# Kernel tuning notes

Hardware: AMD Instinct MI355X
Metric: run time of the kernel (lower is better)

## Reference

```python
import jax, jax.numpy as jnp
import numpy as np

B, L, N, D, TOPK, OUT_V = 32, 512, 1024, 64, 20, 1024
BN_EPS = 1e-5
NEG_SLOPE = 0.2


def setup_inputs() -> dict:
    key = jax.random.key(0)
    ks = jax.random.split(key, 8)
    s = lambda k, shape, sc=0.05: jax.random.normal(k, shape, jnp.float32) * sc
    return {
        "x_enc": jax.random.normal(ks[0], (B, L, N), jnp.float32),
        "emb": s(ks[1], (N, D), 0.1),          # nn.Embedding(variate, d_model).weight
        "lin_W": s(ks[2], (L, D)),              # GraphLayer.lin (no bias)
        "att_i": s(ks[3], (D,)),
        "att_j": s(ks[4], (D,)),
        "att_em_i": s(ks[5], (D,)),
        "att_em_j": s(ks[6], (D,)),
        "gnn_b": jnp.zeros((D,), jnp.float32),  # GraphLayer bias (concat=False)
        "g1": jnp.ones((D,), jnp.float32), "b1": jnp.zeros((D,), jnp.float32),   # GNNLayer.bn
        "g2": jnp.ones((D,), jnp.float32), "b2": jnp.zeros((D,), jnp.float32),   # bn_outlayer_in
        "out_W": s(ks[7], (D, 1)), "out_b": jnp.zeros((1,), jnp.float32),        # OutLayer Linear(d_model, 1)
    }


def _forward(x_enc, emb, lin_W, att_i, att_j, att_em_i, att_em_j,
             gnn_b, g1, b1, g2, b2, out_W, out_b):
    # --- LIN: LayerNorm(input_len, eps=0, no affine) over time, first OUT_V variates ---
    xv = jnp.transpose(x_enc[:, :, :OUT_V], (0, 2, 1))          # [B, OUT_V, L]
    xv = (xv - xv.mean(-1, keepdims=True)) / jnp.sqrt(xv.var(-1, keepdims=True))
    x_enc = x_enc.at[:, :, :OUT_V].set(jnp.transpose(xv, (0, 2, 1)))
    x_enc = jnp.nan_to_num(x_enc, nan=0.0, posinf=0.0, neginf=0.0)

    gt = x_enc[:, -1:, :OUT_V]                                   # [B, 1, OUT_V]
    enc = x_enc.at[:, -1:, :OUT_V].set(0.0)

    # x = enc.transpose(0,1).view(-1, L)  (faithful to original reshape)
    x = jnp.transpose(enc, (1, 0, 2)).reshape(-1, L)             # [B*N, L]

    # --- dynamic top-k cosine-similarity graph (embeddings detached) ---
    w = jax.lax.stop_gradient(emb)
    nrm = jnp.linalg.norm(w, axis=-1)
    cos = (w @ w.T) / (nrm[:, None] * nrm[None, :])              # [N, N]
    topk_idx = jax.lax.top_k(cos, TOPK)[1]                       # [N, TOPK]
    src = topk_idx.reshape(-1)                                   # gated_j (source)
    dst = jnp.repeat(jnp.arange(N), TOPK)                        # gated_i (target)

    offs = (jnp.arange(B) * N)[:, None]
    src_b = (src[None, :] + offs).reshape(-1)                    # [B*N*TOPK]
    dst_b = (dst[None, :] + offs).reshape(-1)

    # remove_self_loops (mask out) then add_self_loops for all B*N nodes
    num_nodes = B * N
    self_mask = jnp.concatenate([src_b == dst_b, jnp.zeros(num_nodes, bool)])
    src_all = jnp.concatenate([src_b, jnp.arange(num_nodes)])
    dst_all = jnp.concatenate([dst_b, jnp.arange(num_nodes)])

    # --- GraphLayer (GAT-style, heads=1, concat=False) ---
    h = x @ lin_W                                                # [B*N, D]
    all_emb = jnp.tile(emb, (B, 1))                              # [B*N, D]

    logit = (h[dst_all] @ att_i + all_emb[dst_all] @ att_em_i
             + h[src_all] @ att_j + all_emb[src_all] @ att_em_j)  # [E]
    logit = jnp.where(logit >= 0, logit, NEG_SLOPE * logit)      # leaky_relu(0.2)
    logit = jnp.where(self_mask, -jnp.inf, logit)

    seg_max = jax.ops.segment_max(logit, dst_all, num_segments=num_nodes)
    expv = jnp.where(self_mask, 0.0, jnp.exp(logit - seg_max[dst_all]))
    denom = jax.ops.segment_sum(expv, dst_all, num_segments=num_nodes)
    alpha = expv / denom[dst_all]

    out = jax.ops.segment_sum(h[src_all] * alpha[:, None], dst_all,
                              num_segments=num_nodes) + gnn_b    # [B*N, D]

    # GNNLayer: BatchNorm1d(D) (batch stats) + ReLU
    out = (out - out.mean(0)) / jnp.sqrt(out.var(0) + BN_EPS) * g1 + b1
    out = jax.nn.relu(out)

    # --- combine with embedding, bn_outlayer_in, OutLayer ---
    xg = out.reshape(B, N, D) * emb[None]                        # [B, N, D]
    xg = jnp.transpose(xg, (0, 2, 1))                            # [B, D, N]
    mu = xg.mean((0, 2), keepdims=True)
    var = xg.var((0, 2), keepdims=True)
    xg = (xg - mu) / jnp.sqrt(var + BN_EPS) * g2[None, :, None] + b2[None, :, None]
    xg = jnp.transpose(jax.nn.relu(xg), (0, 2, 1))               # [B, N, D]

    o = xg @ out_W + out_b                                       # [B, N, 1]
    o = jnp.transpose(o, (0, 2, 1))                              # [B, 1, N]
    return o[:, :, :OUT_V], gt


def reference(x_enc, emb, lin_W, att_i, att_j, att_em_i, att_em_j,
              gnn_b, g1, b1, g2, b2, out_W, out_b):
    return _forward(x_enc, emb, lin_W, att_i, att_j, att_em_i, att_em_j,
                    gnn_b, g1, b1, g2, b2, out_W, out_b)
```

## Files before the change

kernel.cpp:

```cpp
#include <hip/hip_runtime.h>
#include <stdint.h>

#define BB 32
#define LL 512
#define NNODES 1024
#define DD 64
#define TOPK 20
#define NTOT (BB*NNODES)
#define LNSZ (LL*NNODES)

typedef short short8 __attribute__((ext_vector_type(8)));
typedef float floatx4 __attribute__((ext_vector_type(4)));

__device__ __forceinline__ float bf2f(unsigned short u){
    union { unsigned int i; float f; } x; x.i = ((unsigned int)u) << 16; return x.f;
}
__device__ __forceinline__ unsigned short f2bf(float f){
    union { float f; unsigned int i; } x; x.f = f;
    unsigned int u = x.i;
    return (unsigned short)((u + 0x7FFFu + ((u >> 16) & 1u)) >> 16);
}
__device__ __forceinline__ void unpack2(unsigned int w, float& lo, float& hi){
    union { unsigned int i; float f; } a, b;
    a.i = w << 16; b.i = w & 0xFFFF0000u;
    lo = a.f; hi = b.f;
}
__device__ __forceinline__ float ldf(const void* p, int i, int isf){
    return isf ? ((const float*)p)[i] : bf2f(((const unsigned short*)p)[i]);
}
__device__ __forceinline__ int detect_isf(const void* xv){
    const unsigned short* x = (const unsigned short*)xv;
    int lane = threadIdx.x & 63;
    unsigned int idx = ((unsigned)lane * 131071u) & 0x7FFFFFu;
    float v = bf2f(x[idx * 2]);
    float a = fabsf(v);
    int crazy = (!(a <= 1e3f)) || (v != 0.f && a < 1e-6f);
    unsigned long long m = __ballot(crazy);
    return __popcll(m) > 16;
}

__global__ void __launch_bounds__(256) k01_prep(const void* x, const void* lw, unsigned short* wt,
                                                const void* emb, const void* aemi, const void* aemj,
                                                float* eai, float* eaj, float* embT, float* rsqm,
                                                float* part, float* stats){
    int isf = detect_isf(x);
    int t = threadIdx.x;
    if (blockIdx.x == 0) stats[t] = 0.f;
    if (blockIdx.x < 128){
        int id = blockIdx.x * 256 + t;
        int k = id >> 6, d = id & 63;
        unsigned short w = isf ? f2bf(((const float*)lw)[id]) : ((const unsigned short*)lw)[id];
        wt[d * 512 + k] = w;
        {
            int j = id;
            int dd = j >> 10, m = j & 1023;
            embT[j] = ldf(emb, m * 64 + dd, isf);
            j = id + 32768;
            dd = j >> 10; m = j & 1023;
            embT[j] = ldf(emb, m * 64 + dd, isf);
        }
        if (id < 1024){
            int n = id;
            float s1 = 0.f, s2 = 0.f;
            for (int dd = 0; dd < 64; dd++){
                float e = ldf(emb, n * 64 + dd, isf);
                s1 += e * ldf(aemi, dd, isf);
                s2 += e * ldf(aemj, dd, isf);
            }
            eai[n] = s1; eaj[n] = s2;
            float sq = 0.f;
            if (!isf){
                const uint4* pm = (const uint4*)((const unsigned short*)emb + n * 64);
                #pragma unroll
                for (int i = 0; i < 8; i++){
                    uint4 ww = pm[i];
                    float a0,a1,a2,a3,a4,a5,a6,a7;
                    unpack2(ww.x,a0,a1); unpack2(ww.y,a2,a3); unpack2(ww.z,a4,a5); unpack2(ww.w,a6,a7);
                    sq += a0*a0 + a1*a1 + a2*a2 + a3*a3 + a4*a4 + a5*a5 + a6*a6 + a7*a7;
                }
            } else {
                const float4* pm = (const float4*)((const float*)emb + n * 64);
                #pragma unroll
                for (int i = 0; i < 16; i++){
                    float4 ww = pm[i];
                    sq += ww.x*ww.x + ww.y*ww.y + ww.z*ww.z + ww.w*ww.w;
                }
            }
            rsqm[n] = rsqrtf(sq);
        }
    }
    int b = blockIdx.x >> 4, lq = blockIdx.x & 15;
    int n0 = t * 4;
    size_t base = (size_t)b * LNSZ + (size_t)(lq * 32) * NNODES + n0;
    float s0=0,s1=0,s2=0,s3=0,q0=0,q1=0,q2=0,q3=0;
    if (isf){
        const float* p = (const float*)x + base;
        for (int i = 0; i < 32; i++){
            float4 w = *(const float4*)p;
            s0+=w.x; q0+=w.x*w.x; s1+=w.y; q1+=w.y*w.y;
            s2+=w.z; q2+=w.z*w.z; s3+=w.w; q3+=w.w*w.w;
            p += NNODES;
        }
    } else {
        const unsigned short* p = (const unsigned short*)x + base;
        for (int i = 0; i < 32; i++){
            uint2 w = *(const uint2*)p;
            float a,bv,c,d2;
            unpack2(w.x, a, bv); unpack2(w.y, c, d2);
            s0+=a; q0+=a*a; s1+=bv; q1+=bv*bv; s2+=c; q2+=c*c; s3+=d2; q3+=d2*d2;
            p += NNODES;
        }
    }
    int v = b * NNODES + n0;
    float2* pp = (float2*)part;
    pp[(size_t)v*16 + lq]       = make_float2(s0,q0);
    pp[(size_t)(v+1)*16 + lq]   = make_float2(s1,q1);
    pp[(size_t)(v+2)*16 + lq]   = make_float2(s2,q2);
    pp[(size_t)(v+3)*16 + lq]   = make_float2(s3,q3);
}

__global__ void __launch_bounds__(256) k13_topk(const void* emb, const float* embT, const float* rsqm,
                                                int* topk, const void* x, const float* part,
                                                float* mr, float* outp){
    __shared__ float enf[64];
    __shared__ float n2s;
    __shared__ float crow[1024];
    int isf = detect_isf(x);
    int wave = threadIdx.x >> 6, lane = threadIdx.x & 63;
    int n = blockIdx.x;
    if (blockIdx.x < 128){
        int v = blockIdx.x * 256 + threadIdx.x;
        const float2* pp = (const float2*)part + (size_t)v * 16;
        float s = 0.f, q = 0.f;
        for (int i = 0; i < 16; i++){ float2 w = pp[i]; s += w.x; q += w.y; }
        float mean = s * (1.f/512.f);
        float var  = q * (1.f/512.f) - mean * mean;
        float rstd = var > 0.f ? rsqrtf(var) : 0.f;
        ((float2*)mr)[v] = make_float2(mean, rstd);
        int b = v >> 10, nn = v & 1023;
        float xv = ldf(x, (int)((size_t)b * LNSZ + (size_t)511 * NNODES + nn), isf);
        outp[NTOT + v] = (xv - mean) * rstd;
    }
    if (wave == 0){
        float e = ldf(emb, n * 64 + lane, isf);
        enf[lane] = e;
        float p1 = e * e;
        #pragma unroll
        for (int m = 1; m < 64; m <<= 1) p1 += __shfl_xor(p1, m, 64);
        if (lane == 0) n2s = p1;
    }
    __syncthreads();
    float rn_own = rsqrtf(n2s);
    const float* en = enf;
    int mb = wave * 256 + lane * 4;
    float dot0 = 0.f, dot1 = 0.f, dot2 = 0.f, dot3 = 0.f;
    if (!isf){
        #pragma unroll
        for (int i = 0; i < 8; i++){
            float4 a0 = *(const float4*)(embT + (i*8+0)*1024 + mb);
            float4 a1 = *(const float4*)(embT + (i*8+1)*1024 + mb);
            float4 a2 = *(const float4*)(embT + (i*8+2)*1024 + mb);
            float4 a3 = *(const float4*)(embT + (i*8+3)*1024 + mb);
            float4 a4 = *(const float4*)(embT + (i*8+4)*1024 + mb);
            float4 a5 = *(const float4*)(embT + (i*8+5)*1024 + mb);
            float4 a6 = *(const float4*)(embT + (i*8+6)*1024 + mb);
            float4 a7 = *(const float4*)(embT + (i*8+7)*1024 + mb);
            const float* e8 = en + i * 8;
            dot0 += e8[0]*a0.x + e8[1]*a1.x + e8[2]*a2.x + e8[3]*a3.x
                  + e8[4]*a4.x + e8[5]*a5.x + e8[6]*a6.x + e8[7]*a7.x;
            dot1 += e8[0]*a0.y + e8[1]*a1.y + e8[2]*a2.y + e8[3]*a3.y
                  + e8[4]*a4.y + e8[5]*a5.y + e8[6]*a6.y + e8[7]*a7.y;
            dot2 += e8[0]*a0.z + e8[1]*a1.z + e8[2]*a2.z + e8[3]*a3.z
                  + e8[4]*a4.z + e8[5]*a5.z + e8[6]*a6.z + e8[7]*a7.z;
            dot3 += e8[0]*a0.w + e8[1]*a1.w + e8[2]*a2.w + e8[3]*a3.w
                  + e8[4]*a4.w + e8[5]*a5.w + e8[6]*a6.w + e8[7]*a7.w;
        }
    } else {
        #pragma unroll
        for (int i = 0; i < 16; i++){
            float4 a0 = *(const float4*)(embT + (i*4+0)*1024 + mb);
            float4 a1 = *(const float4*)(embT + (i*4+1)*1024 + mb);
            float4 a2 = *(const float4*)(embT + (i*4+2)*1024 + mb);
            float4 a3 = *(const float4*)(embT + (i*4+3)*1024 + mb);
            const float* e4 = en + i * 4;
            dot0 += e4[0]*a0.x + e4[1]*a1.x + e4[2]*a2.x + e4[3]*a3.x;
            dot1 += e4[0]*a0.y + e4[1]*a1.y + e4[2]*a2.y + e4[3]*a3.y;
            dot2 += e4[0]*a0.z + e4[1]*a1.z + e4[2]*a2.z + e4[3]*a3.z;
            dot3 += e4[0]*a0.w + e4[1]*a1.w + e4[2]*a2.w + e4[3]*a3.w;
        }
    }
    crow[mb+0] = dot0 * rn_own * rsqm[mb+0];
    crow[mb+1] = dot1 * rn_own * rsqm[mb+1];
    crow[mb+2] = dot2 * rn_own * rsqm[mb+2];
    crow[mb+3] = dot3 * rn_own * rsqm[mb+3];
    __syncthreads();
    if (wave != 0) return;
    float va[16];
    #pragma unroll
    for (int ii = 0; ii < 16; ii++) va[ii] = crow[ii * 64 + lane];
    for (int k = 0; k < TOPK; k++){
        float t8[8]; int x8[8];
        #pragma unroll
        for (int j = 0; j < 8; j++){
            bool c = va[2*j+1] > va[2*j];
            t8[j] = c ? va[2*j+1] : va[2*j]; x8[j] = c ? 2*j+1 : 2*j;
        }
        #pragma unroll
        for (int j = 0; j < 4; j++){
            bool c = t8[2*j+1] > t8[2*j];
            t8[j] = c ? t8[2*j+1] : t8[2*j]; x8[j] = c ? x8[2*j+1] : x8[2*j];
        }
        #pragma unroll
        for (int j = 0; j < 2; j++){
            bool c = t8[2*j+1] > t8[2*j];
            t8[j] = c ? t8[2*j+1] : t8[2*j]; x8[j] = c ? x8[2*j+1] : x8[2*j];
        }
        bool c0 = t8[1] > t8[0];
        float bv = c0 ? t8[1] : t8[0]; int bi = c0 ? x8[1] : x8[0];
        int bm = bi * 64 + lane;
        #pragma unroll
        for (int s = 1; s < 64; s <<= 1){
            float ov = __shfl_xor(bv, s, 64);
            int   om = __shfl_xor(bm, s, 64);
            bool u = (ov > bv) || (ov == bv && om < bm);
            bv = u ? ov : bv; bm = u ? om : bm;
        }
        if (lane == 0) topk[n * TOPK + k] = bm;
        int evi = bm >> 6;
        bool own = ((bm & 63) == lane);
        #pragma unroll
        for (int ii = 0; ii < 16; ii++)
            va[ii] = (own && ii == evi) ? -__builtin_inff() : va[ii];
    }
}

__global__ void __launch_bounds__(256) k2_gemm_h(const void* x, const unsigned short* wt,
                                                const float* mr, unsigned short* hb,
                                                const void* atti, const void* attj,
                                                const float* eai, const float* eaj,
                                                float* ai, float* aj){
    __shared__ unsigned short A_l[64 * 136];
    __shared__ unsigned short W_l[64 * 136];
    __shared__ float4 colp4[256];
    int isf = detect_isf(x);
    int t = threadIdx.x;
    int q = blockIdx.x & 63, mtile = blockIdx.x >> 6;
    int b = q >> 1, nbase = (q & 1) * 512;
    size_t xbase = (size_t)b * LNSZ + nbase;

    colp4[t] = ((const float4*)mr)[q * 256 + t];

    int wave = t >> 6, lane = t & 63;
    int quad = lane >> 4, lcol = lane & 15;
    floatx4 acc[4];
    for (int j = 0; j < 4; j++) acc[j] = (floatx4){0.f,0.f,0.f,0.f};
    __syncthreads();

    for (int kc = 0; kc < 4; kc++){
        for (int i = 0; i < 4; i++){
            int id = i * 256 + t;
            int l = id >> 4, c16 = id & 15;
            int lg = mtile * 64 + l;
            uint4 o;
            if (lg == 511){
                o = make_uint4(0u, 0u, 0u, 0u);
            } else {
                size_t ofs = xbase + (size_t)lg * NNODES + kc * 128 + c16 * 8;
                float e0,e1,e2,e3,e4,e5,e6,e7;
                if (isf){
                    const float4* px = (const float4*)((const float*)x + ofs);
                    float4 wa = px[0], wb = px[1];
                    e0=wa.x; e1=wa.y; e2=wa.z; e3=wa.w; e4=wb.x; e5=wb.y; e6=wb.z; e7=wb.w;
                } else {
                    uint4 w = *(const uint4*)((const unsigned short*)x + ofs);
                    unpack2(w.x,e0,e1); unpack2(w.y,e2,e3); unpack2(w.z,e4,e5); unpack2(w.w,e6,e7);
                }
                int f4b = kc * 64 + c16 * 4;
                float4 pA = colp4[f4b+0], pB = colp4[f4b+1], pC = colp4[f4b+2], pD = colp4[f4b+3];
                e0 = (e0 - pA.x) * pA.y;  e1 = (e1 - pA.z) * pA.w;
                e2 = (e2 - pB.x) * pB.y;  e3 = (e3 - pB.z) * pB.w;
                e4 = (e4 - pC.x) * pC.y;  e5 = (e5 - pC.z) * pC.w;
                e6 = (e6 - pD.x) * pD.y;  e7 = (e7 - pD.z) * pD.w;
                o.x = (unsigned)f2bf(e0) | ((unsigned)f2bf(e1) << 16);
                o.y = (unsigned)f2bf(e2) | ((unsigned)f2bf(e3) << 16);
                o.z = (unsigned)f2bf(e4) | ((unsigned)f2bf(e5) << 16);
                o.w = (unsigned)f2bf(e6) | ((unsigned)f2bf(e7) << 16);
            }
            *(uint4*)&A_l[l * 136 + c16 * 8] = o;
        }
        for (int i = 0; i < 4; i++){
            int id = i * 256 + t;
            int dd = id >> 4, c16 = id & 15;
            uint4 w = *(const uint4*)(wt + dd * 512 + kc * 128 + c16 * 8);
            *(uint4*)&W_l[dd * 136 + c16 * 8] = w;
        }
        __syncthreads();
        for (int ks = 0; ks < 4; ks++){
            short8 af, bfr[4];
            af = *(const short8*)&A_l[(wave * 16 + lcol) * 136 + ks * 32 + quad * 8];
            for (int tc = 0; tc < 4; tc++)
                bfr[tc] = *(const short8*)&W_l[(tc * 16 + lcol) * 136 + ks * 32 + quad * 8];
            for (int tc = 0; tc < 4; tc++)
                acc[tc] = __builtin_amdgcn_mfma_f32_16x16x32_bf16(af, bfr[tc], acc[tc], 0, 0, 0);
        }
        __syncthreads();
    }
    float aw[4], jw[4];
    #pragma unroll
    for (int tc = 0; tc < 4; tc++){
        int dcol = tc * 16 + lcol;
        aw[tc] = ldf(atti, dcol, isf);
        jw[tc] = ldf(attj, dcol, isf);
    }
    #pragma unroll
    for (int r = 0; r < 4; r++){
        float pi = 0.f, pj = 0.f;
        #pragma unroll
        for (int tc = 0; tc < 4; tc++){
            float hv = acc[tc][r];
            pi += hv * aw[tc];
            pj += hv * jw[tc];
        }
        #pragma unroll
        for (int s = 1; s < 16; s <<= 1){
            pi += __shfl_xor(pi, s, 64);
            pj += __shfl_xor(pj, s, 64);
        }
        if (lcol == 0){
            int lrow = wave * 16 + quad * 4 + r;
            int row = (mtile * 64 + lrow) * 64 + q;
            int n = row & 1023;
            ai[row] = pi + eai[n];
            aj[row] = pj + eaj[n];
        }
    }
    for (int tc = 0; tc < 4; tc++){
        int dcol = tc * 16 + lcol;
        for (int r = 0; r < 4; r++){
            int lrow = wave * 16 + quad * 4 + r;
            int row = (mtile * 64 + lrow) * 64 + q;
            hb[(size_t)row * 64 + dcol] = f2bf(acc[tc][r]);
        }
    }
}

__global__ void __launch_bounds__(256) k5_attn(const unsigned short* hb, const float* ai, const float* aj,
                                               const int* topk, const void* gnn_b, float* out, const void* x){
    int isf = detect_isf(x);
    int wave = threadIdx.x >> 6, lane = threadIdx.x & 63;
    float gb = ldf(gnn_b, lane, isf);
    int v = blockIdx.x * 4 + wave;
    int n = v & 1023, bbase = v & ~1023;
    int srcv; bool valid;
    if (lane < TOPK){
        int id = topk[n * TOPK + lane];
        srcv = bbase | id;
        valid = (id != n);
    } else if (lane == TOPK){
        srcv = v; valid = true;
    } else { srcv = v; valid = false; }
    float l = ai[v] + aj[srcv];
    l = (l >= 0.f) ? l : 0.2f * l;
    if (!valid) l = -__builtin_inff();
    float m = l;
    #pragma unroll
    for (int s = 1; s < 64; s <<= 1){ float o = __shfl_xor(m, s, 64); m = fmaxf(m, o); }
    float ev = valid ? __expf(l - m) : 0.f;
    float dsum = ev;
    #pragma unroll
    for (int s = 1; s < 64; s <<= 1) dsum += __shfl_xor(dsum, s, 64);
    float rd = 1.f / dsum;
    float acc = 0.f;
    #pragma unroll
    for (int j = 0; j <= TOPK; j++){
        float e = __shfl(ev, j, 64);
        int  sj = __shfl(srcv, j, 64);
        acc += e * bf2f(hb[(size_t)sj * 64 + lane]);
    }
    out[(size_t)v * 64 + lane] = acc * rd + gb;
}

__global__ void __launch_bounds__(256) k5b_stats(const float* out, float* stats1){
    __shared__ float bs[256], bq[256];
    int wave = threadIdx.x >> 6, lane = threadIdx.x & 63;
    int v0 = blockIdx.x * 128 + wave * 32;
    float ssum = 0.f, ssq = 0.f;
    for (int i = 0; i < 32; i++){
        float x = out[(size_t)(v0 + i) * 64 + lane];
        ssum += x; ssq += x * x;
    }
    bs[threadIdx.x] = ssum; bq[threadIdx.x] = ssq;
    __syncthreads();
    if (wave == 0){
        float s  = bs[lane] + bs[64+lane] + bs[128+lane] + bs[192+lane];
        float qq = bq[lane] + bq[64+lane] + bq[128+lane] + bq[192+lane];
        atomicAdd(&stats1[lane], s);
        atomicAdd(&stats1[64 + lane], qq);
    }
}

__global__ void __launch_bounds__(256) k6_stats2(const float* out, const float* stats1, const void* g1,
                                                 const void* b1, const void* emb,
                                                 float* stats2, const void* x){
    __shared__ float bs[256], bq[256];
    int isf = detect_isf(x);
    int wave = threadIdx.x >> 6, lane = threadIdx.x & 63;
    float mu   = stats1[lane] * (1.f/32768.f);
    float var  = stats1[64 + lane] * (1.f/32768.f) - mu * mu;
    float rstd = 1.f / sqrtf(var + 1e-5f);
    float g = ldf(g1, lane, isf), bb = ldf(b1, lane, isf);
    float ssum = 0.f, ssq = 0.f;
    int v0 = (blockIdx.x * 4 + wave) * 16;
    for (int i = 0; i < 16; i++){
        int v = v0 + i; int n = v & 1023;
        float xv = out[(size_t)v * 64 + lane];
        float y = fmaxf((xv - mu) * rstd * g + bb, 0.f);
        float z = y * ldf(emb, n * 64 + lane, isf);
        ssum += z; ssq += z * z;
    }
    bs[threadIdx.x] = ssum; bq[threadIdx.x] = ssq;
    __syncthreads();
    if (wave == 0){
        float s  = bs[lane] + bs[64+lane] + bs[128+lane] + bs[192+lane];
        float qq = bq[lane] + bq[64+lane] + bq[128+lane] + bq[192+lane];
        atomicAdd(&stats2[lane], s);
        atomicAdd(&stats2[64 + lane], qq);
    }
}

__global__ void __launch_bounds__(256) k7_out(const float* out, const float* stats1, const float* stats2,
                                              const void* g1, const void* b1,
                                              const void* g2, const void* b2,
                                              const void* emb, const void* outw,
                                              const void* outb, float* o, const void* x){
    int isf = detect_isf(x);
    int wave = threadIdx.x >> 6, lane = threadIdx.x & 63;
    float mu1   = stats1[lane] * (1.f/32768.f);
    float var1  = stats1[64 + lane] * (1.f/32768.f) - mu1 * mu1;
    float rstd1 = 1.f / sqrtf(var1 + 1e-5f);
    float g1v = ldf(g1, lane, isf), b1v = ldf(b1, lane, isf);
    float mu2   = stats2[lane] * (1.f/32768.f);
    float var2  = stats2[64 + lane] * (1.f/32768.f) - mu2 * mu2;
    float rstd2 = 1.f / sqrtf(var2 + 1e-5f);
    float g2v = ldf(g2, lane, isf), b2v = ldf(b2, lane, isf);
    float w = ldf(outw, lane, isf);
    float ob = ldf(outb, 0, isf);
    int v0 = (blockIdx.x * 4 + wave) * 16;
    for (int i = 0; i < 16; i++){
        int v = v0 + i; int n = v & 1023;
        float xv = out[(size_t)v * 64 + lane];
        float z = fmaxf((xv - mu1) * rstd1 * g1v + b1v, 0.f) * ldf(emb, n * 64 + lane, isf);
        float y = fmaxf((z - mu2) * rstd2 * g2v + b2v, 0.f);
        float p = y * w;
        for (int s = 1; s < 64; s <<= 1) p += __shfl_xor(p, s, 64);
        if (lane == 0) o[v] = p + ob;
    }
}

extern "C" void kernel_launch(void* const* d_in, const int* in_sizes, int n_in,
                              void* d_out, int out_size, void* d_ws, size_t ws_size,
                              hipStream_t stream){
    const void* x    = d_in[0];
    const void* emb  = d_in[1];
    const void* linW = d_in[2];
    const void* atti = d_in[3];
    const void* attj = d_in[4];
    const void* aemi = d_in[5];
    const void* aemj = d_in[6];
    const void* gnnb = d_in[7];
    const void* g1   = d_in[8];
    const void* b1   = d_in[9];
    const void* g2   = d_in[10];
    const void* b2   = d_in[11];
    const void* outw = d_in[12];
    const void* outb = d_in[13];
    float* o = (float*)d_out;

    char* w = (char*)d_ws;
    float*          mr    = (float*)(w + 0);
    unsigned short* wt    = (unsigned short*)(w + 262144);
    unsigned short* hb    = (unsigned short*)(w + 327680);
    float*          eai   = (float*)(w + 8716288);
    float*          eaj   = (float*)(w + 8720384);
    int*            topk  = (int*)(w + 8724480);
    float*          ai    = (float*)(w + 8806400);
    float*          aj    = (float*)(w + 8937472);
    float*          outg  = (float*)(w + 9068544);
    float*          part  = outg;
    float*          embT  = (float*)(w + 13262848);
    float*          rsqm  = (float*)(w + 13524992);
    float*          stats = (float*)(w + 17457152);

    hipLaunchKernelGGL(k01_prep, dim3(512),  dim3(256), 0, stream, x, linW, wt, emb, aemi, aemj,
                       eai, eaj, embT, rsqm, part, stats);
    hipLaunchKernelGGL(k13_topk, dim3(1024), dim3(256), 0, stream, emb, embT, rsqm, topk, x, part, mr, o);
    hipLaunchKernelGGL(k2_gemm_h, dim3(512), dim3(256), 0, stream, x, wt, mr, hb, atti, attj, eai, eaj, ai, aj);
    hipLaunchKernelGGL(k5_attn,  dim3(8192), dim3(256), 0, stream, hb, ai, aj, topk, gnnb, outg, x);
    hipLaunchKernelGGL(k5b_stats, dim3(256), dim3(256), 0, stream, outg, stats);
    hipLaunchKernelGGL(k6_stats2, dim3(512), dim3(256), 0, stream, outg, stats, g1, b1, emb, stats + 128, x);
    hipLaunchKernelGGL(k7_out,   dim3(512),  dim3(256), 0, stream, outg, stats, stats + 128,
                       g1, b1, g2, b2, emb, outw, outb, o, x);
}
```

Before: 233.4 us.

## Load GEMM fragments directly from global memory into registers, dropping LDS staging

The k2_gemm_h kernel no longer stages the normalized input tile and weight tile through shared memory with block barriers. Each lane now loads its own MFMA A fragment directly from global memory, applies the per-column normalization inline, and reads the B fragments directly from the weight array, with the loops fully unrolled. This removes LDS writes and reads and the __syncthreads barriers. In exchange, the weight tile is re-read from global/L2 by every wave rather than shared once per block, and the global access patterns are less coalesced, since each lane reads 8 contiguous elements from a different row.

```diff
diff --git a/kernel.cpp b/kernel.cpp
--- a/kernel.cpp
+++ b/kernel.cpp
@@ -239,33 +239,28 @@
                                                 const void* atti, const void* attj,
                                                 const float* eai, const float* eaj,
                                                 float* ai, float* aj){
-    __shared__ unsigned short A_l[64 * 136];
-    __shared__ unsigned short W_l[64 * 136];
-    __shared__ float4 colp4[256];
     int isf = detect_isf(x);
     int t = threadIdx.x;
     int q = blockIdx.x & 63, mtile = blockIdx.x >> 6;
     int b = q >> 1, nbase = (q & 1) * 512;
     size_t xbase = (size_t)b * LNSZ + nbase;
-
-    colp4[t] = ((const float4*)mr)[q * 256 + t];
-
     int wave = t >> 6, lane = t & 63;
     int quad = lane >> 4, lcol = lane & 15;
+    int lg = mtile * 64 + wave * 16 + lcol;
+    const float4* colp = (const float4*)mr + q * 256;
+
     floatx4 acc[4];
+    #pragma unroll
     for (int j = 0; j < 4; j++) acc[j] = (floatx4){0.f,0.f,0.f,0.f};
-    __syncthreads();
 
     for (int kc = 0; kc < 4; kc++){
-        for (int i = 0; i < 4; i++){
-            int id = i * 256 + t;
-            int l = id >> 4, c16 = id & 15;
-            int lg = mtile * 64 + l;
-            uint4 o;
+        short8 af[4];
+        #pragma unroll
+        for (int ks = 0; ks < 4; ks++){
             if (lg == 511){
-                o = make_uint4(0u, 0u, 0u, 0u);
+                af[ks] = (short8){0,0,0,0,0,0,0,0};
             } else {
-                size_t ofs = xbase + (size_t)lg * NNODES + kc * 128 + c16 * 8;
+                size_t ofs = xbase + (size_t)lg * NNODES + kc * 128 + ks * 32 + quad * 8;
                 float e0,e1,e2,e3,e4,e5,e6,e7;
                 if (isf){
                     const float4* px = (const float4*)((const float*)x + ofs);
@@ -275,35 +270,30 @@
                     uint4 w = *(const uint4*)((const unsigned short*)x + ofs);
                     unpack2(w.x,e0,e1); unpack2(w.y,e2,e3); unpack2(w.z,e4,e5); unpack2(w.w,e6,e7);
                 }
-                int f4b = kc * 64 + c16 * 4;
-                float4 pA = colp4[f4b+0], pB = colp4[f4b+1], pC = colp4[f4b+2], pD = colp4[f4b+3];
+                int f = kc * 64 + ks * 16 + quad * 4;
+                float4 pA = colp[f], pB = colp[f+1], pC = colp[f+2], pD = colp[f+3];
                 e0 = (e0 - pA.x) * pA.y;  e1 = (e1 - pA.z) * pA.w;
                 e2 = (e2 - pB.x) * pB.y;  e3 = (e3 - pB.z) * pB.w;
                 e4 = (e4 - pC.x) * pC.y;  e5 = (e5 - pC.z) * pC.w;
                 e6 = (e6 - pD.x) * pD.y;  e7 = (e7 - pD.z) * pD.w;
-                o.x = (unsigned)f2bf(e0) | ((unsigned)f2bf(e1) << 16);
-                o.y = (unsigned)f2bf(e2) | ((unsigned)f2bf(e3) << 16);
-                o.z = (unsigned)f2bf(e4) | ((unsigned)f2bf(e5) << 16);
-                o.w = (unsigned)f2bf(e6) | ((unsigned)f2bf(e7) << 16);
+                short8 a;
+                a[0] = (short)f2bf(e0); a[1] = (short)f2bf(e1);
+                a[2] = (short)f2bf(e2); a[3] = (short)f2bf(e3);
+                a[4] = (short)f2bf(e4); a[5] = (short)f2bf(e5);
+                a[6] = (short)f2bf(e6); a[7] = (short)f2bf(e7);
+                af[ks] = a;
             }
-            *(uint4*)&A_l[l * 136 + c16 * 8] = o;
-        }
-        for (int i = 0; i < 4; i++){
-            int id = i * 256 + t;
-            int dd = id >> 4, c16 = id & 15;
-            uint4 w = *(const uint4*)(wt + dd * 512 + kc * 128 + c16 * 8);
-            *(uint4*)&W_l[dd * 136 + c16 * 8] = w;
-        }
-        __syncthreads();
+        }
+        #pragma unroll
         for (int ks = 0; ks < 4; ks++){
-            short8 af, bfr[4];
-            af = *(const short8*)&A_l[(wave * 16 + lcol) * 136 + ks * 32 + quad * 8];
+            short8 bfr[4];
+            #pragma unroll
             for (int tc = 0; tc < 4; tc++)
-                bfr[tc] = *(const short8*)&W_l[(tc * 16 + lcol) * 136 + ks * 32 + quad * 8];
+                bfr[tc] = *(const short8*)(wt + (tc * 16 + lcol) * 512 + kc * 128 + ks * 32 + quad * 8);
+            #pragma unroll
             for (int tc = 0; tc < 4; tc++)
-                acc[tc] = __builtin_amdgcn_mfma_f32_16x16x32_bf16(af, bfr[tc], acc[tc], 0, 0, 0);
-        }
-        __syncthreads();
+                acc[tc] = __builtin_amdgcn_mfma_f32_16x16x32_bf16(af[ks], bfr[tc], acc[tc], 0, 0, 0);
+        }
     }
     float aw[4], jw[4];
     #pragma unroll
@@ -334,8 +324,10 @@
             aj[row] = pj + eaj[n];
         }
     }
+    #pragma unroll
     for (int tc = 0; tc < 4; tc++){
         int dcol = tc * 16 + lcol;
+        #pragma unroll
         for (int r = 0; r < 4; r++){
             int lrow = wave * 16 + quad * 4 + r;
             int row = (mtile * 64 + lrow) * 64 + q;
```

Result: slower. 248.1 us (+6.3%).

## Widen stats reduction grid, transpose partial layout, swizzle GEMM shared tiles

Applied to the files above, without the earlier changes.

The per-variate LayerNorm statistics pass now runs on twice as many blocks, with each thread reading 8 contiguous variates over 8 time steps. Partial sums go into a partition-major layout so both the writes and the reads in the topk kernel are coalesced. The GEMM kernel replaces its padded shared-memory tiles with XOR-swizzled uint4 tiles to avoid bank conflicts without padding, and unrolls its loops. The reducer now sums 64 partials instead of 16, and part moves to a separate workspace region, which assumes the workspace is large enough.

```diff
diff --git a/kernel.cpp b/kernel.cpp
--- a/kernel.cpp
+++ b/kernel.cpp
@@ -89,34 +89,46 @@
             rsqm[n] = rsqrtf(sq);
         }
     }
-    int b = blockIdx.x >> 4, lq = blockIdx.x & 15;
-    int n0 = t * 4;
-    size_t base = (size_t)b * LNSZ + (size_t)(lq * 32) * NNODES + n0;
-    float s0=0,s1=0,s2=0,s3=0,q0=0,q1=0,q2=0,q3=0;
+    int b = blockIdx.x >> 5, lq = blockIdx.x & 31;
+    int th = t & 127, rh = t >> 7;
+    int n0 = th * 8;
+    int l0 = lq * 16 + rh * 8;
+    size_t base = (size_t)b * LNSZ + (size_t)l0 * NNODES + n0;
+    float s0=0,s1=0,s2=0,s3=0,s4=0,s5=0,s6=0,s7=0;
+    float q0=0,q1=0,q2=0,q3=0,q4=0,q5=0,q6=0,q7=0;
     if (isf){
         const float* p = (const float*)x + base;
-        for (int i = 0; i < 32; i++){
-            float4 w = *(const float4*)p;
-            s0+=w.x; q0+=w.x*w.x; s1+=w.y; q1+=w.y*w.y;
-            s2+=w.z; q2+=w.z*w.z; s3+=w.w; q3+=w.w*w.w;
+        #pragma unroll
+        for (int i = 0; i < 8; i++){
+            float4 wa = *(const float4*)p;
+            float4 wb = *(const float4*)(p + 4);
+            s0+=wa.x; q0+=wa.x*wa.x; s1+=wa.y; q1+=wa.y*wa.y;
+            s2+=wa.z; q2+=wa.z*wa.z; s3+=wa.w; q3+=wa.w*wa.w;
+            s4+=wb.x; q4+=wb.x*wb.x; s5+=wb.y; q5+=wb.y*wb.y;
+            s6+=wb.z; q6+=wb.z*wb.z; s7+=wb.w; q7+=wb.w*wb.w;
             p += NNODES;
         }
     } else {
         const unsigned short* p = (const unsigned short*)x + base;
-        for (int i = 0; i < 32; i++){
-            uint2 w = *(const uint2*)p;
-            float a,bv,c,d2;
-            unpack2(w.x, a, bv); unpack2(w.y, c, d2);
-            s0+=a; q0+=a*a; s1+=bv; q1+=bv*bv; s2+=c; q2+=c*c; s3+=d2; q3+=d2*d2;
+        #pragma unroll
+        for (int i = 0; i < 8; i++){
+            uint4 w = *(const uint4*)p;
+            float e0,e1,e2,e3,e4,e5,e6,e7;
+            unpack2(w.x,e0,e1); unpack2(w.y,e2,e3); unpack2(w.z,e4,e5); unpack2(w.w,e6,e7);
+            s0+=e0; q0+=e0*e0; s1+=e1; q1+=e1*e1;
+            s2+=e2; q2+=e2*e2; s3+=e3; q3+=e3*e3;
+            s4+=e4; q4+=e4*e4; s5+=e5; q5+=e5*e5;
+            s6+=e6; q6+=e6*e6; s7+=e7; q7+=e7*e7;
             p += NNODES;
         }
     }
-    int v = b * NNODES + n0;
-    float2* pp = (float2*)part;
-    pp[(size_t)v*16 + lq]       = make_float2(s0,q0);
-    pp[(size_t)(v+1)*16 + lq]   = make_float2(s1,q1);
-    pp[(size_t)(v+2)*16 + lq]   = make_float2(s2,q2);
-    pp[(size_t)(v+3)*16 + lq]   = make_float2(s3,q3);
+    int pidx = lq * 2 + rh;
+    int v = b * 1024 + n0;
+    float2* pp = (float2*)part + (size_t)pidx * 32768 + v;
+    pp[0]=make_float2(s0,q0); pp[1]=make_float2(s1,q1);
+    pp[2]=make_float2(s2,q2); pp[3]=make_float2(s3,q3);
+    pp[4]=make_float2(s4,q4); pp[5]=make_float2(s5,q5);
+    pp[6]=make_float2(s6,q6); pp[7]=make_float2(s7,q7);
 }
 
 __global__ void __launch_bounds__(256) k13_topk(const void* emb, const float* embT, const float* rsqm,
@@ -130,9 +142,11 @@
     int n = blockIdx.x;
     if (blockIdx.x < 128){
         int v = blockIdx.x * 256 + threadIdx.x;
-        const float2* pp = (const float2*)part + (size_t)v * 16;
         float s = 0.f, q = 0.f;
-        for (int i = 0; i < 16; i++){ float2 w = pp[i]; s += w.x; q += w.y; }
+        for (int i = 0; i < 64; i++){
+            float2 w = ((const float2*)part)[(size_t)i * 32768 + v];
+            s += w.x; q += w.y;
+        }
         float mean = s * (1.f/512.f);
         float var  = q * (1.f/512.f) - mean * mean;
         float rstd = var > 0.f ? rsqrtf(var) : 0.f;
@@ -239,8 +253,8 @@
                                                 const void* atti, const void* attj,
                                                 const float* eai, const float* eaj,
                                                 float* ai, float* aj){
-    __shared__ unsigned short A_l[64 * 136];
-    __shared__ unsigned short W_l[64 * 136];
+    __shared__ uint4 A4[64 * 16];
+    __shared__ uint4 W4[64 * 16];
     __shared__ float4 colp4[256];
     int isf = detect_isf(x);
     int t = threadIdx.x;
@@ -257,6 +271,7 @@
     __syncthreads();
 
     for (int kc = 0; kc < 4; kc++){
+        #pragma unroll
         for (int i = 0; i < 4; i++){
             int id = i * 256 + t;
             int l = id >> 4, c16 = id & 15;
@@ -286,20 +301,26 @@
                 o.z = (unsigned)f2bf(e4) | ((unsigned)f2bf(e5) << 16);
                 o.w = (unsigned)f2bf(e6) | ((unsigned)f2bf(e7) << 16);
             }
-            *(uint4*)&A_l[l * 136 + c16 * 8] = o;
-        }
+            A4[l * 16 + (c16 ^ (l & 15))] = o;
+        }
+        #pragma unroll
         for (int i = 0; i < 4; i++){
             int id = i * 256 + t;
             int dd = id >> 4, c16 = id & 15;
             uint4 w = *(const uint4*)(wt + dd * 512 + kc * 128 + c16 * 8);
-            *(uint4*)&W_l[dd * 136 + c16 * 8] = w;
+            W4[dd * 16 + (c16 ^ (dd & 15))] = w;
         }
         __syncthreads();
+        #pragma unroll
         for (int ks = 0; ks < 4; ks++){
-            short8 af, bfr[4];
-            af = *(const short8*)&A_l[(wave * 16 + lcol) * 136 + ks * 32 + quad * 8];
+            int cx = ks * 4 + quad;
+            int arow = wave * 16 + lcol;
+            short8 af = *(const short8*)&A4[arow * 16 + (cx ^ lcol)];
+            short8 bfr[4];
+            #pragma unroll
             for (int tc = 0; tc < 4; tc++)
-                bfr[tc] = *(const short8*)&W_l[(tc * 16 + lcol) * 136 + ks * 32 + quad * 8];
+                bfr[tc] = *(const short8*)&W4[(tc * 16 + lcol) * 16 + (cx ^ lcol)];
+            #pragma unroll
             for (int tc = 0; tc < 4; tc++)
                 acc[tc] = __builtin_amdgcn_mfma_f32_16x16x32_bf16(af, bfr[tc], acc[tc], 0, 0, 0);
         }
@@ -334,8 +355,10 @@
             aj[row] = pj + eaj[n];
         }
     }
+    #pragma unroll
     for (int tc = 0; tc < 4; tc++){
         int dcol = tc * 16 + lcol;
+        #pragma unroll
         for (int r = 0; r < 4; r++){
             int lrow = wave * 16 + quad * 4 + r;
             int row = (mtile * 64 + lrow) * 64 + q;
@@ -486,12 +509,12 @@
     float*          ai    = (float*)(w + 8806400);
     float*          aj    = (float*)(w + 8937472);
     float*          outg  = (float*)(w + 9068544);
-    float*          part  = outg;
     float*          embT  = (float*)(w + 13262848);
     float*          rsqm  = (float*)(w + 13524992);
     float*          stats = (float*)(w + 17457152);
-
-    hipLaunchKernelGGL(k01_prep, dim3(512),  dim3(256), 0, stream, x, linW, wt, emb, aemi, aemj,
+    float*          part  = (float*)(w + 18874368);
+
+    hipLaunchKernelGGL(k01_prep, dim3(1024), dim3(256), 0, stream, x, linW, wt, emb, aemi, aemj,
                        eai, eaj, embT, rsqm, part, stats);
     hipLaunchKernelGGL(k13_topk, dim3(1024), dim3(256), 0, stream, emb, embT, rsqm, topk, x, part, mr, o);
     hipLaunchKernelGGL(k2_gemm_h, dim3(512), dim3(256), 0, stream, x, wt, mr, hb, atti, attj, eai, eaj, ai, aj);
```

After: 237.5 us. No clear change (+1.7%).
